# Kernel optimization log

Hardware: AMD Instinct MI355X
Metric: run time of the kernel (lower is better)

The kernel has to match this reference:

```python
import jax, jax.numpy as jnp
import numpy as np

B, T, C, H = 2, 2048, 1024, 16
NS, NL, STEP = 3, 1, 8            # n_s_token, n_l_token, online_step
NPF = NS + NL                      # tokens per frame
CHUNK = STEP * NPF                 # online chunk size = 32
D = C // H


def _build_causal_mask():
    # Faithful port of the buffer construction in __init__ (host-side numpy).
    m = np.tril(np.ones((T, T), dtype=np.float32))
    step = np.zeros((T, T), dtype=np.float32)
    for i in range(0, T, CHUNK):
        step[i:i + CHUNK, i:i + CHUNK] = 1.0
        for j in range(i, i + CHUNK, NPF):
            m[j + NS:j + NPF, :] = 0.0
            m[:, j + NS:j + NPF] = 0.0
    return jnp.asarray(((m + step) == 0.0))[None, None]  # (1,1,T,T) bool


def setup_inputs() -> dict:
    key = jax.random.key(0)
    ks = jax.random.split(key, 10)
    sc = 0.02
    return {
        "x": jax.random.normal(ks[0], (B, T, C), dtype=jnp.float32),
        "dynamic_mask": jax.random.randint(ks[1], (B, 1, T, T), 0, 2).astype(bool),
        "causal_mask": _build_causal_mask(),
        "Wq": jax.random.normal(ks[2], (C, C), dtype=jnp.float32) * sc,
        "bq": jnp.zeros((C,), dtype=jnp.float32),
        "Wk": jax.random.normal(ks[3], (C, C), dtype=jnp.float32) * sc,
        "bk": jnp.zeros((C,), dtype=jnp.float32),
        "Wv": jax.random.normal(ks[4], (C, C), dtype=jnp.float32) * sc,
        "bv": jnp.zeros((C,), dtype=jnp.float32),
        "Wo": jax.random.normal(ks[5], (C, C), dtype=jnp.float32) * sc,
        "bo": jnp.zeros((C,), dtype=jnp.float32),
    }


def reference(x, dynamic_mask, causal_mask, Wq, bq, Wk, bk, Wv, bv, Wo, bo):
    Bb, Tt, Cc = x.shape
    scale = jnp.asarray(D, x.dtype) ** -0.5
    # nn.Linear: y = x @ W.T + b ; split heads -> (B,H,T,D)
    q = (x @ Wq.T + bq).reshape(Bb, Tt, H, D).transpose(0, 2, 1, 3)
    k = (x @ Wk.T + bk).reshape(Bb, Tt, H, D).transpose(0, 2, 1, 3)
    v = (x @ Wv.T + bv).reshape(Bb, Tt, H, D).transpose(0, 2, 1, 3)
    att = jnp.einsum('bhqd,bhkd->bhqk', q, k) * scale       # (B,H,T,T)
    neg_inf = jnp.asarray(-jnp.inf, att.dtype)
    att = jnp.where(causal_mask, neg_inf, att)
    att = jnp.where(dynamic_mask, neg_inf, att)
    att = jax.nn.softmax(att, axis=-1)                      # attn_drop is identity (eval)
    y = jnp.einsum('bhqk,bhkd->bhqd', att, v)
    y = y.transpose(0, 2, 1, 3).reshape(Bb, Tt, Cc)
    return y @ Wo.T + bo                                    # resid_drop is identity (eval)
```

## Files before the change

### kernel.cpp

```cpp
#include <hip/hip_runtime.h>

#define TSEQ 2048
#define NHEAD 16
#define DHEAD 64
#define CDIM 1024
#define BATCH 2

typedef __attribute__((ext_vector_type(8))) short bfx8;
typedef __attribute__((ext_vector_type(4))) short bfx4;
typedef __attribute__((ext_vector_type(4))) float f32x4;

__device__ __forceinline__ unsigned short f2bf(float f) {
  unsigned u = __builtin_bit_cast(unsigned, f);
  u += 0x7fffu + ((u >> 16) & 1u);
  return (unsigned short)(u >> 16);
}

__device__ __forceinline__ unsigned cvtpk(float lo, float hi) {
  unsigned r;
  asm("v_cvt_pk_bf16_f32 %0, %1, %2" : "=v"(r) : "v"(lo), "v"(hi));
  return r;
}

__device__ __forceinline__ float max3f(float a, float b, float c) {
  float d;
  asm("v_max3_f32 %0, %1, %2, %3" : "=v"(d) : "v"(a), "v"(b), "v"(c));
  return d;
}

__device__ __forceinline__ void gload16(const void* g, void* l) {
  __builtin_amdgcn_global_load_lds(
      (const __attribute__((address_space(1))) unsigned*)g,
      (__attribute__((address_space(3))) unsigned*)l, 16, 0, 0);
}

__global__ __launch_bounds__(256) void prep(
    const float* __restrict__ x,
    const float* __restrict__ wq, const float* __restrict__ wk,
    const float* __restrict__ wv, const float* __restrict__ wo,
    short* __restrict__ xb, short* __restrict__ wall,
    const unsigned char* __restrict__ dyn,
    const unsigned char* __restrict__ causal,
    unsigned long long* __restrict__ pm) {
  const int bid = blockIdx.x;
  if (bid < 20480) {
    const int y = bid >> 12;
    const float* src;
    short* dst;
    int n;
    if (y == 0) { src = x; dst = xb; n = (BATCH * TSEQ * CDIM) / 4; }
    else {
      src = (y == 1) ? wq : (y == 2) ? wk : (y == 3) ? wv : wo;
      dst = wall + (size_t)(y - 1) * CDIM * CDIM;
      n = (CDIM * CDIM) / 4;
    }
    const int i = (bid & 4095) * 256 + threadIdx.x;
    if (i < n) {
      const float4 v = ((const float4*)src)[i];
      bfx4 o;
      o[0] = (short)f2bf(v.x); o[1] = (short)f2bf(v.y);
      o[2] = (short)f2bf(v.z); o[3] = (short)f2bf(v.w);
      ((bfx4*)dst)[i] = o;
    }
  } else {
    const bool mbyte = (causal[32] != 0);
    const int wave = threadIdx.x >> 6, lane = threadIdx.x & 63;
    const int gid = (bid - 20480) * 4 + wave;
    const int tile = gid & 31;
    const int q = (gid >> 5) & (TSEQ - 1);
    const int b = gid >> 16;
    const int g = lane >> 4, blk = (lane >> 2) & 3, r = lane & 3;
    const int k = tile * 64 + blk * 16 + g * 4 + r;
    const size_t off = ((size_t)b * TSEQ + q) * TSEQ + k;
    const bool dm = mbyte ? (dyn[off] != 0) : (((const int*)dyn)[off] != 0);
    const bool qok = (q & 3) != 3;
    const bool al =
        (((k >> 5) == (q >> 5)) || ((k <= q) && qok && (r != 3))) && !dm;
    const unsigned long long bal = __ballot(!al);
    if (lane == 0) pm[gid] = bal;
  }
}

__global__ __launch_bounds__(256) void gemm_qkv(
    const short* __restrict__ A, const short* __restrict__ Ball,
    const float* __restrict__ bias0, const float* __restrict__ bias1,
    const float* __restrict__ bias2,
    short* __restrict__ Oq, short* __restrict__ Ok, short* __restrict__ VT) {
  __shared__ char arena[35072];
  const int bid = blockIdx.x;
  const int xcd = bid & 7, local = bid >> 3;
  const int m_idx = (xcd >> 1) * 8 + (local & 7);
  const int nz = (xcd & 1) * 12 + (local >> 3);
  const int which = nz >> 3, n_idx = nz & 7;
  const int tid = threadIdx.x;
  const int w = tid >> 6, lane = tid & 63;
  const int lq = lane & 15, g = lane >> 4;
  const int wr = w >> 1, wc = w & 1;
  const int m0 = m_idx * 128, n0 = n_idx * 128;
  const short* B = Ball + (size_t)which * CDIM * CDIM;
#define ASB(bi) ((short*)(arena + (bi) * 8192))
#define BSB(bi) ((short*)(arena + 16384 + (bi) * 8192))
#define GS(bi, kt)                                                             \
  {                                                                            \
    _Pragma("unroll") for (int ph = 0; ph < 2; ++ph) {                         \
      const int c = ph * 256 + tid;                                            \
      gload16(A + (size_t)(m0 + (c >> 2)) * CDIM + (kt) * 32 + (c & 3) * 8,    \
              ASB(bi) + (ph * 256 + w * 64) * 8);                              \
      gload16(B + (size_t)(n0 + (c >> 2)) * CDIM + (kt) * 32 + (c & 3) * 8,    \
              BSB(bi) + (ph * 256 + w * 64) * 8);                              \
    }                                                                          \
  }
  GS(0, 0);
  __syncthreads();
  f32x4 acc[4][4] = {};
#pragma unroll 2
  for (int kt = 0; kt < CDIM / 32; ++kt) {
    const int bi = kt & 1;
    if (kt + 1 < CDIM / 32) GS(bi ^ 1, kt + 1);
    bfx8 af[4], bfr[4];
#pragma unroll
    for (int i = 0; i < 4; ++i)
      af[i] = *(const bfx8*)&ASB(bi)[(wr * 64 + i * 16 + lq) * 32 + g * 8];
#pragma unroll
    for (int i = 0; i < 4; ++i)
      bfr[i] = *(const bfx8*)&BSB(bi)[(wc * 64 + i * 16 + lq) * 32 + g * 8];
#pragma unroll
    for (int i = 0; i < 4; ++i)
#pragma unroll
      for (int j = 0; j < 4; ++j)
        acc[i][j] = __builtin_amdgcn_mfma_f32_16x16x32_bf16(af[i], bfr[j],
                                                            acc[i][j], 0, 0, 0);
    __syncthreads();
  }
#undef GS
  const float* bias = (which == 0) ? bias0 : (which == 1) ? bias1 : bias2;
  const float scale = (which == 0) ? 0.18033688011112042f : 1.0f;
  short* tile = (short*)arena;
  const int rs = (which == 2) ? 137 : 136;
#pragma unroll
  for (int i = 0; i < 4; ++i)
#pragma unroll
    for (int j = 0; j < 4; ++j) {
      const int col = wc * 64 + j * 16 + lq;
      const float bb = bias[n0 + col];
#pragma unroll
      for (int r = 0; r < 4; ++r) {
        const int row = wr * 64 + i * 16 + g * 4 + r;
        tile[row * rs + col] = (short)f2bf((acc[i][j][r] + bb) * scale);
      }
    }
  __syncthreads();
  const int b_ = m0 >> 11, t0 = m0 & (TSEQ - 1);
  if (which == 2) {
#pragma unroll
    for (int it = 0; it < 8; ++it) {
      const int id = it * 256 + tid;
      const int tseg = id & 15, d128 = id >> 4;
      const int h = (n0 >> 6) + (d128 >> 6), d = d128 & 63;
      bfx8 o;
#pragma unroll
      for (int j = 0; j < 8; ++j) o[j] = tile[(tseg * 8 + j) * 137 + d128];
      *(bfx8*)&VT[(((size_t)b_ * NHEAD + h) * DHEAD + d) * TSEQ + t0 +
                  tseg * 8] = o;
    }
  } else {
    short* O = (which == 0) ? Oq : Ok;
#pragma unroll
    for (int it = 0; it < 8; ++it) {
      const int id = it * 256 + tid;
      const int m = id >> 4, c16 = id & 15;
      const int h = (n0 >> 6) + (c16 >> 3), d0 = (c16 & 7) * 8;
      *(bfx8*)&O[(((size_t)b_ * NHEAD + h) * TSEQ + t0 + m) * DHEAD + d0] =
          *(const bfx8*)&tile[m * 136 + c16 * 8];
    }
  }
}

__global__ __launch_bounds__(256) void gemm_out(
    const short* __restrict__ A, const short* __restrict__ B,
    const float* __restrict__ bias, float* __restrict__ Of) {
  __shared__ char arena[24576];
  const int bid = blockIdx.x;
  const int xcd = bid & 7, local = bid >> 3;
  const int m_idx = (xcd >> 1) * 16 + (local & 15);
  const int n_idx = (xcd & 1) * 4 + (local >> 4);
  const int tid = threadIdx.x;
  const int w = tid >> 6, lane = tid & 63;
  const int lq = lane & 15, g = lane >> 4;
  const int wr = w >> 1, wc = w & 1;
  const int m0 = m_idx * 64, n0 = n_idx * 128;
#define ASB(bi) ((short*)(arena + (bi) * 4096))
#define BSB(bi) ((short*)(arena + 8192 + (bi) * 8192))
#define GS(bi, kt)                                                             \
  {                                                                            \
    gload16(A + (size_t)(m0 + (tid >> 2)) * CDIM + (kt) * 32 + (tid & 3) * 8,  \
            ASB(bi) + (w * 64) * 8);                                           \
    _Pragma("unroll") for (int ph = 0; ph < 2; ++ph) {                         \
      const int c = ph * 256 + tid;                                            \
      gload16(B + (size_t)(n0 + (c >> 2)) * CDIM + (kt) * 32 + (c & 3) * 8,    \
              BSB(bi) + (ph * 256 + w * 64) * 8);                              \
    }                                                                          \
  }
  GS(0, 0);
  __syncthreads();
  f32x4 acc[2][4] = {};
#pragma unroll 2
  for (int kt = 0; kt < CDIM / 32; ++kt) {
    const int bi = kt & 1;
    if (kt + 1 < CDIM / 32) GS(bi ^ 1, kt + 1);
    bfx8 af[2], bfr[4];
#pragma unroll
    for (int i = 0; i < 2; ++i)
      af[i] = *(const bfx8*)&ASB(bi)[(wr * 32 + i * 16 + lq) * 32 + g * 8];
#pragma unroll
    for (int j = 0; j < 4; ++j)
      bfr[j] = *(const bfx8*)&BSB(bi)[(wc * 64 + j * 16 + lq) * 32 + g * 8];
#pragma unroll
    for (int i = 0; i < 2; ++i)
#pragma unroll
      for (int j = 0; j < 4; ++j)
        acc[i][j] = __builtin_amdgcn_mfma_f32_16x16x32_bf16(af[i], bfr[j],
                                                            acc[i][j], 0, 0, 0);
    __syncthreads();
  }
#undef GS
#undef ASB
#undef BSB
#pragma unroll
  for (int i = 0; i < 2; ++i)
#pragma unroll
    for (int j = 0; j < 4; ++j) {
      const int col = n0 + wc * 64 + j * 16 + lq;
      const float bb = bias[col];
#pragma unroll
      for (int r = 0; r < 4; ++r) {
        const int row = m0 + wr * 32 + i * 16 + g * 4 + r;
        Of[(size_t)row * CDIM + col] = acc[i][j][r] + bb;
      }
    }
}

struct QPhase {
  bfx8 qf0, qf1;
  f32x4 acc[4];
  float m, l;
  const unsigned short* pmr;
};

__device__ __forceinline__ void attn_half(QPhase& S, const char* kbuf,
                                          const char* vbuf, short* Pw,
                                          unsigned mb, int hf, int sw, int lq,
                                          int g) {
  f32x4 st[2] = {};
  __builtin_amdgcn_s_setprio(1);
#pragma unroll
  for (int b2 = 0; b2 < 2; ++b2) {
    const int rowb = ((hf * 2 + b2) * 16 + lq) * 128;
    const bfx8 kf0 = *(const bfx8*)&kbuf[rowb + ((g * 16) ^ sw)];
    const bfx8 kf1 = *(const bfx8*)&kbuf[rowb + ((64 + g * 16) ^ sw)];
    st[b2] =
        __builtin_amdgcn_mfma_f32_16x16x32_bf16(kf0, S.qf0, st[b2], 0, 0, 0);
    st[b2] =
        __builtin_amdgcn_mfma_f32_16x16x32_bf16(kf1, S.qf1, st[b2], 0, 0, 0);
  }
  __builtin_amdgcn_s_setprio(0);
  float s8[8];
#pragma unroll
  for (int idx = 0; idx < 8; ++idx)
    s8[idx] = ((mb >> idx) & 1u) ? -3.0e38f : st[idx >> 2][idx & 3];
  const float t0 = max3f(s8[0], s8[1], s8[2]);
  const float t1 = max3f(s8[3], s8[4], s8[5]);
  const float pmax = max3f(t0, t1, fmaxf(s8[6], s8[7]));
  if (!__all(pmax - S.m <= 8.f)) {
    float smax = fmaxf(pmax, __shfl_xor(pmax, 16));
    smax = fmaxf(smax, __shfl_xor(smax, 32));
    const float mnew = fmaxf(S.m, smax);
    const float fac = __builtin_amdgcn_exp2f(S.m - mnew);
    S.l *= fac;
    float fr[4];
#pragma unroll
    for (int r = 0; r < 4; ++r) fr[r] = __shfl(fac, g * 4 + r);
#pragma unroll
    for (int dc = 0; dc < 4; ++dc) {
      S.acc[dc][0] *= fr[0]; S.acc[dc][1] *= fr[1];
      S.acc[dc][2] *= fr[2]; S.acc[dc][3] *= fr[3];
    }
    S.m = mnew;
  }
  float psum = 0.f;
#pragma unroll
  for (int idx = 0; idx < 8; ++idx) {
    const float e = __builtin_amdgcn_exp2f(s8[idx] - S.m);
    s8[idx] = e;
    psum += e;
  }
  S.l += psum;
#pragma unroll
  for (int b2 = 0; b2 < 2; ++b2) {
    uint2 u;
    u.x = cvtpk(s8[b2 * 4 + 0], s8[b2 * 4 + 1]);
    u.y = cvtpk(s8[b2 * 4 + 2], s8[b2 * 4 + 3]);
    *(uint2*)&Pw[lq * 40 + b2 * 16 + g * 4] = u;
  }
  __builtin_amdgcn_wave_barrier();
  const bfx8 pa = *(const bfx8*)&Pw[lq * 40 + g * 8];
  __builtin_amdgcn_wave_barrier();
  __builtin_amdgcn_s_setprio(1);
#pragma unroll
  for (int dc = 0; dc < 4; ++dc) {
    const bfx8 vf = *(const bfx8*)&vbuf[(dc * 16 + lq) * 128 +
                                        ((hf * 64 + g * 16) ^ sw)];
    S.acc[dc] =
        __builtin_amdgcn_mfma_f32_16x16x32_bf16(pa, vf, S.acc[dc], 0, 0, 0);
  }
  __builtin_amdgcn_s_setprio(0);
}

__global__ __launch_bounds__(512, 4) void attn(
    const short* __restrict__ Q, const short* __restrict__ K,
    const short* __restrict__ VT, const unsigned short* __restrict__ pm,
    short* __restrict__ Y) {
  __shared__ char arena[43008];
  const int bid = blockIdx.x;
  const int local = bid >> 3;
  const int bh = (bid & 7) * 4 + (local >> 4);
  const int tlo = local & 15, thi = 31 - tlo;
  const int tid = threadIdx.x;
  const int w = tid >> 6, lane = tid & 63;
  const int hf = w >> 2, ws = w & 3;
  const int lq = lane & 15, g = lane >> 4;
  const int b = bh >> 4, h = bh & 15;
  const short* Qb = Q + (size_t)bh * TSEQ * DHEAD;
  const short* Kb = K + (size_t)bh * TSEQ * DHEAD;
  const short* Vb = VT + (size_t)bh * DHEAD * TSEQ;

  QPhase lo, hi;
  {
    const int qlo = tlo * 64 + ws * 16 + lq;
    const int qhi = thi * 64 + ws * 16 + lq;
    lo.qf0 = *(const bfx8*)(Qb + (size_t)qlo * DHEAD + g * 8);
    lo.qf1 = *(const bfx8*)(Qb + (size_t)qlo * DHEAD + 32 + g * 8);
    hi.qf0 = *(const bfx8*)(Qb + (size_t)qhi * DHEAD + g * 8);
    hi.qf1 = *(const bfx8*)(Qb + (size_t)qhi * DHEAD + 32 + g * 8);
#pragma unroll
    for (int dc = 0; dc < 4; ++dc) { lo.acc[dc] = f32x4{}; hi.acc[dc] = f32x4{}; }
    lo.m = -1e30f; lo.l = 0.f; hi.m = -1e30f; hi.l = 0.f;
    lo.pmr = pm + ((size_t)(b * TSEQ + qlo) << 7) + g;
    hi.pmr = pm + ((size_t)(b * TSEQ + qhi) << 7) + g;
  }

  const int sl = lane >> 3, sc = lane & 7;
  const int ssw = (sc ^ sl) * 8;
  const int sw = (lq & 7) << 4;
  short* Pw = (short*)(arena + 32768 + w * 1280);

#define STAGE(bufn, k0s)                                                      \
  {                                                                           \
    gload16(Kb + (size_t)((k0s) + w * 8 + sl) * DHEAD + ssw,                  \
            arena + (bufn) * 16384 + w * 1024);                               \
    gload16(Vb + (size_t)(w * 8 + sl) * TSEQ + (k0s) + ssw,                   \
            arena + (bufn) * 16384 + 8192 + w * 1024);                        \
  }

#define PHASE(t, BUF)                                                         \
  {                                                                           \
    const unsigned pmh = hi.pmr[(t) << 2];                                    \
    const unsigned pml = ((t) <= tlo) ? (unsigned)lo.pmr[(t) << 2] : 0u;      \
    __builtin_amdgcn_sched_barrier(0);                                        \
    if ((t) < thi) STAGE((BUF) ^ 1, ((t) + 1) * 64);                          \
    const char* kbuf_ = arena + (BUF) * 16384;                                \
    const char* vbuf_ = kbuf_ + 8192;                                         \
    attn_half(hi, kbuf_, vbuf_, Pw, (pmh >> (hf * 8)) & 0xffu, hf, sw, lq, g);\
    if ((t) <= tlo)                                                           \
      attn_half(lo, kbuf_, vbuf_, Pw, (pml >> (hf * 8)) & 0xffu, hf, sw, lq,  \
                g);                                                           \
    __syncthreads();                                                          \
  }

  STAGE(0, 0);
  __syncthreads();

  int t = 0;
  for (; t + 1 <= thi; t += 2) {
    PHASE(t, 0);
    PHASE(t + 1, 1);
  }
  if (t <= thi) PHASE(t, 0);
#undef PHASE
#undef STAGE

  float* exA = (float*)arena;
  float2* exM = (float2*)(arena + 32768);
  if (hf == 1) {
#pragma unroll
    for (int ph = 0; ph < 2; ++ph) {
      QPhase& S = ph ? hi : lo;
      float* a = exA + (ws * 2 + ph) * 1024;
#pragma unroll
      for (int dc = 0; dc < 4; ++dc)
        *(f32x4*)&a[lane * 16 + dc * 4] = S.acc[dc];
      exM[(ws * 2 + ph) * 64 + lane] = float2{S.m, S.l};
    }
  }
  __syncthreads();
  if (hf == 0) {
#pragma unroll
    for (int ph = 0; ph < 2; ++ph) {
      QPhase& S = ph ? hi : lo;
      const float* a = exA + (ws * 2 + ph) * 1024;
      const float2 mlB = exM[(ws * 2 + ph) * 64 + lane];
      const float ms = fmaxf(S.m, mlB.x);
      const float fA = __builtin_amdgcn_exp2f(S.m - ms);
      const float fB = __builtin_amdgcn_exp2f(mlB.x - ms);
      float lr = S.l * fA + mlB.y * fB;
      lr += __shfl_xor(lr, 16);
      lr += __shfl_xor(lr, 32);
      float frA[4], frB[4], li[4];
#pragma unroll
      for (int r = 0; r < 4; ++r) {
        frA[r] = __shfl(fA, g * 4 + r);
        frB[r] = __shfl(fB, g * 4 + r);
        const float lv = __shfl(lr, g * 4 + r);
        li[r] = lv > 0.f ? 1.f / lv : 0.f;
      }
      const int q0 = (ph ? thi : tlo) * 64 + ws * 16;
#pragma unroll
      for (int dc = 0; dc < 4; ++dc) {
        const f32x4 ab = *(const f32x4*)&a[lane * 16 + dc * 4];
#pragma unroll
        for (int r = 0; r < 4; ++r) {
          const int t2 = q0 + g * 4 + r;
          Y[((size_t)b * TSEQ + t2) * CDIM + h * DHEAD + dc * 16 + lq] =
              (short)f2bf((S.acc[dc][r] * frA[r] + ab[r] * frB[r]) * li[r]);
        }
      }
    }
  }
}

extern "C" void kernel_launch(void* const* d_in, const int* in_sizes, int n_in,
                              void* d_out, int out_size, void* d_ws,
                              size_t ws_size, hipStream_t stream) {
  const float* x = (const float*)d_in[0];
  const unsigned char* dyn = (const unsigned char*)d_in[1];
  const unsigned char* causal = (const unsigned char*)d_in[2];
  const float* Wq = (const float*)d_in[3];
  const float* bq = (const float*)d_in[4];
  const float* Wk = (const float*)d_in[5];
  const float* bk = (const float*)d_in[6];
  const float* Wv = (const float*)d_in[7];
  const float* bv = (const float*)d_in[8];
  const float* Wo = (const float*)d_in[9];
  const float* bo = (const float*)d_in[10];

  char* ws = (char*)d_ws;
  const size_t MB8 = 8ull * 1024 * 1024;
  short* xb = (short*)(ws + 0 * MB8);
  short* wall = (short*)(ws + 1 * MB8);
  short* Qb = (short*)(ws + 2 * MB8);
  short* Kb = (short*)(ws + 3 * MB8);
  short* VTb = (short*)(ws + 5 * MB8);
  short* Yb = (short*)(ws + 6 * MB8);
  unsigned long long* pmask = (unsigned long long*)(ws + 7 * MB8);

  prep<<<dim3(53248), 256, 0, stream>>>(x, Wq, Wk, Wv, Wo, xb, wall, dyn,
                                        causal, pmask);
  gemm_qkv<<<dim3(768), 256, 0, stream>>>(xb, wall, bq, bk, bv, Qb, Kb, VTb);
  attn<<<dim3(512), 512, 0, stream>>>(Qb, Kb, VTb,
                                      (const unsigned short*)pmask, Yb);
  gemm_out<<<dim3(512), 256, 0, stream>>>(Yb, wall + 3 * CDIM * CDIM, bo,
                                          (float*)d_out);
}
```

Measured before the change: 122.5 us.

## Split paired lo/hi query tiles into separate blocks with staggered scheduling

The attention kernel previously had each block process two query tiles (a low and a high one) to balance causal work. Now each block handles a single 64-row query tile, the grid doubles to 1024 blocks, and the tile index is permuted across four block-row groups so short and long tiles interleave. The per-block register footprint and LDS drop: one QPhase state, P scratch stride shrinks from 40 to 32, and launch bounds rise to allow more resident blocks. The intended gain is higher occupancy and better latency hiding. The cost is losing the shared K/V reuse between the two tiles and risking load imbalance and LDS bank conflicts with the unpadded P stride.

```diff
diff --git a/kernel.cpp b/kernel.cpp
--- a/kernel.cpp
+++ b/kernel.cpp
@@ -300,10 +300,10 @@
     uint2 u;
     u.x = cvtpk(s8[b2 * 4 + 0], s8[b2 * 4 + 1]);
     u.y = cvtpk(s8[b2 * 4 + 2], s8[b2 * 4 + 3]);
-    *(uint2*)&Pw[lq * 40 + b2 * 16 + g * 4] = u;
+    *(uint2*)&Pw[lq * 32 + b2 * 16 + g * 4] = u;
   }
   __builtin_amdgcn_wave_barrier();
-  const bfx8 pa = *(const bfx8*)&Pw[lq * 40 + g * 8];
+  const bfx8 pa = *(const bfx8*)&Pw[lq * 32 + g * 8];
   __builtin_amdgcn_wave_barrier();
   __builtin_amdgcn_s_setprio(1);
 #pragma unroll
@@ -316,15 +316,17 @@
   __builtin_amdgcn_s_setprio(0);
 }
 
-__global__ __launch_bounds__(512, 4) void attn(
+__global__ __launch_bounds__(512, 8) void attn(
     const short* __restrict__ Q, const short* __restrict__ K,
     const short* __restrict__ VT, const unsigned short* __restrict__ pm,
     short* __restrict__ Y) {
-  __shared__ char arena[43008];
+  __shared__ char arena[40960];
   const int bid = blockIdx.x;
-  const int local = bid >> 3;
-  const int bh = (bid & 7) * 4 + (local >> 4);
-  const int tlo = local & 15, thi = 31 - tlo;
+  const int x = bid & 255, y = bid >> 8;
+  const int p = x >> 3;
+  const int bh = (x & 7) * 4 + y;
+  const int r5 = (p + 5) & 31;
+  const int qb = (y == 0) ? p : (y == 1) ? (31 - p) : (y == 2) ? r5 : (31 - r5);
   const int tid = threadIdx.x;
   const int w = tid >> 6, lane = tid & 63;
   const int hf = w >> 2, ws = w & 3;
@@ -334,25 +336,22 @@
   const short* Kb = K + (size_t)bh * TSEQ * DHEAD;
   const short* Vb = VT + (size_t)bh * DHEAD * TSEQ;
 
-  QPhase lo, hi;
+  QPhase S;
   {
-    const int qlo = tlo * 64 + ws * 16 + lq;
-    const int qhi = thi * 64 + ws * 16 + lq;
-    lo.qf0 = *(const bfx8*)(Qb + (size_t)qlo * DHEAD + g * 8);
-    lo.qf1 = *(const bfx8*)(Qb + (size_t)qlo * DHEAD + 32 + g * 8);
-    hi.qf0 = *(const bfx8*)(Qb + (size_t)qhi * DHEAD + g * 8);
-    hi.qf1 = *(const bfx8*)(Qb + (size_t)qhi * DHEAD + 32 + g * 8);
-#pragma unroll
-    for (int dc = 0; dc < 4; ++dc) { lo.acc[dc] = f32x4{}; hi.acc[dc] = f32x4{}; }
-    lo.m = -1e30f; lo.l = 0.f; hi.m = -1e30f; hi.l = 0.f;
-    lo.pmr = pm + ((size_t)(b * TSEQ + qlo) << 7) + g;
-    hi.pmr = pm + ((size_t)(b * TSEQ + qhi) << 7) + g;
+    const int q = qb * 64 + ws * 16 + lq;
+    S.qf0 = *(const bfx8*)(Qb + (size_t)q * DHEAD + g * 8);
+    S.qf1 = *(const bfx8*)(Qb + (size_t)q * DHEAD + 32 + g * 8);
+#pragma unroll
+    for (int dc = 0; dc < 4; ++dc) S.acc[dc] = f32x4{};
+    S.m = -1e30f;
+    S.l = 0.f;
+    S.pmr = pm + ((size_t)(b * TSEQ + q) << 7) + g;
   }
 
   const int sl = lane >> 3, sc = lane & 7;
   const int ssw = (sc ^ sl) * 8;
   const int sw = (lq & 7) << 4;
-  short* Pw = (short*)(arena + 32768 + w * 1280);
+  short* Pw = (short*)(arena + 32768 + w * 1024);
 
 #define STAGE(bufn, k0s)                                                      \
   {                                                                           \
@@ -364,16 +363,12 @@
 
 #define PHASE(t, BUF)                                                         \
   {                                                                           \
-    const unsigned pmh = hi.pmr[(t) << 2];                                    \
-    const unsigned pml = ((t) <= tlo) ? (unsigned)lo.pmr[(t) << 2] : 0u;      \
+    const unsigned pmw = S.pmr[(t) << 2];                                     \
     __builtin_amdgcn_sched_barrier(0);                                        \
-    if ((t) < thi) STAGE((BUF) ^ 1, ((t) + 1) * 64);                          \
+    if ((t) < qb) STAGE((BUF) ^ 1, ((t) + 1) * 64);                           \
     const char* kbuf_ = arena + (BUF) * 16384;                                \
     const char* vbuf_ = kbuf_ + 8192;                                         \
-    attn_half(hi, kbuf_, vbuf_, Pw, (pmh >> (hf * 8)) & 0xffu, hf, sw, lq, g);\
-    if ((t) <= tlo)                                                           \
-      attn_half(lo, kbuf_, vbuf_, Pw, (pml >> (hf * 8)) & 0xffu, hf, sw, lq,  \
-                g);                                                           \
+    attn_half(S, kbuf_, vbuf_, Pw, (pmw >> (hf * 8)) & 0xffu, hf, sw, lq, g); \
     __syncthreads();                                                          \
   }
 
@@ -381,58 +376,49 @@
   __syncthreads();
 
   int t = 0;
-  for (; t + 1 <= thi; t += 2) {
+  for (; t + 1 <= qb; t += 2) {
     PHASE(t, 0);
     PHASE(t + 1, 1);
   }
-  if (t <= thi) PHASE(t, 0);
+  if (t <= qb) PHASE(t, 0);
 #undef PHASE
 #undef STAGE
 
   float* exA = (float*)arena;
-  float2* exM = (float2*)(arena + 32768);
+  float2* exM = (float2*)(arena + 16384);
   if (hf == 1) {
-#pragma unroll
-    for (int ph = 0; ph < 2; ++ph) {
-      QPhase& S = ph ? hi : lo;
-      float* a = exA + (ws * 2 + ph) * 1024;
-#pragma unroll
-      for (int dc = 0; dc < 4; ++dc)
-        *(f32x4*)&a[lane * 16 + dc * 4] = S.acc[dc];
-      exM[(ws * 2 + ph) * 64 + lane] = float2{S.m, S.l};
-    }
+    float* a = exA + ws * 1024;
+#pragma unroll
+    for (int dc = 0; dc < 4; ++dc) *(f32x4*)&a[lane * 16 + dc * 4] = S.acc[dc];
+    exM[ws * 64 + lane] = float2{S.m, S.l};
   }
   __syncthreads();
   if (hf == 0) {
-#pragma unroll
-    for (int ph = 0; ph < 2; ++ph) {
-      QPhase& S = ph ? hi : lo;
-      const float* a = exA + (ws * 2 + ph) * 1024;
-      const float2 mlB = exM[(ws * 2 + ph) * 64 + lane];
-      const float ms = fmaxf(S.m, mlB.x);
-      const float fA = __builtin_amdgcn_exp2f(S.m - ms);
-      const float fB = __builtin_amdgcn_exp2f(mlB.x - ms);
-      float lr = S.l * fA + mlB.y * fB;
-      lr += __shfl_xor(lr, 16);
-      lr += __shfl_xor(lr, 32);
-      float frA[4], frB[4], li[4];
+    const float* a = exA + ws * 1024;
+    const float2 mlB = exM[ws * 64 + lane];
+    const float ms = fmaxf(S.m, mlB.x);
+    const float fA = __builtin_amdgcn_exp2f(S.m - ms);
+    const float fB = __builtin_amdgcn_exp2f(mlB.x - ms);
+    float lr = S.l * fA + mlB.y * fB;
+    lr += __shfl_xor(lr, 16);
+    lr += __shfl_xor(lr, 32);
+    float frA[4], frB[4], li[4];
+#pragma unroll
+    for (int r = 0; r < 4; ++r) {
+      frA[r] = __shfl(fA, g * 4 + r);
+      frB[r] = __shfl(fB, g * 4 + r);
+      const float lv = __shfl(lr, g * 4 + r);
+      li[r] = lv > 0.f ? 1.f / lv : 0.f;
+    }
+    const int q0 = qb * 64 + ws * 16;
+#pragma unroll
+    for (int dc = 0; dc < 4; ++dc) {
+      const f32x4 ab = *(const f32x4*)&a[lane * 16 + dc * 4];
 #pragma unroll
       for (int r = 0; r < 4; ++r) {
-        frA[r] = __shfl(fA, g * 4 + r);
-        frB[r] = __shfl(fB, g * 4 + r);
-        const float lv = __shfl(lr, g * 4 + r);
-        li[r] = lv > 0.f ? 1.f / lv : 0.f;
-      }
-      const int q0 = (ph ? thi : tlo) * 64 + ws * 16;
-#pragma unroll
-      for (int dc = 0; dc < 4; ++dc) {
-        const f32x4 ab = *(const f32x4*)&a[lane * 16 + dc * 4];
-#pragma unroll
-        for (int r = 0; r < 4; ++r) {
-          const int t2 = q0 + g * 4 + r;
-          Y[((size_t)b * TSEQ + t2) * CDIM + h * DHEAD + dc * 16 + lq] =
-              (short)f2bf((S.acc[dc][r] * frA[r] + ab[r] * frB[r]) * li[r]);
-        }
+        const int t2 = q0 + g * 4 + r;
+        Y[((size_t)b * TSEQ + t2) * CDIM + h * DHEAD + dc * 16 + lq] =
+            (short)f2bf((S.acc[dc][r] * frA[r] + ab[r] * frB[r]) * li[r]);
       }
     }
   }
@@ -466,8 +452,8 @@
   prep<<<dim3(53248), 256, 0, stream>>>(x, Wq, Wk, Wv, Wo, xb, wall, dyn,
                                         causal, pmask);
   gemm_qkv<<<dim3(768), 256, 0, stream>>>(xb, wall, bq, bk, bv, Qb, Kb, VTb);
-  attn<<<dim3(512), 512, 0, stream>>>(Qb, Kb, VTb,
-                                      (const unsigned short*)pmask, Yb);
+  attn<<<dim3(1024), 512, 0, stream>>>(Qb, Kb, VTb,
+                                       (const unsigned short*)pmask, Yb);
   gemm_out<<<dim3(512), 256, 0, stream>>>(Yb, wall + 3 * CDIM * CDIM, bo,
                                           (float*)d_out);
 }
```

After: 143.6 us. 1.17x slower.
